# Optimization experiments

Measured on AMD Instinct MI355X. Metric: run time of the kernel, lower is better.

Reference implementation:

```python
import jax, jax.numpy as jnp
import numpy as np

N = 100000   # nodes
E = 1600000  # edges (avg degree 16)
D = 128      # input_dim == output_dim (residual requires equality)
BN_EPS = 1e-5


def setup_inputs() -> dict:
    key = jax.random.key(0)
    ks = jax.random.split(key, 8)
    X = jax.random.normal(ks[0], (N, D), dtype=jnp.float32)
    E_X = jax.random.normal(ks[1], (E, D), dtype=jnp.float32)
    snorm_n = jax.random.uniform(ks[2], (N, 1), dtype=jnp.float32)
    snorm_e = jax.random.uniform(ks[3], (E, 1), dtype=jnp.float32)
    src = jax.random.randint(ks[4], (E,), 0, N, dtype=jnp.int32)
    dst = jax.random.randint(ks[5], (E,), 0, N, dtype=jnp.int32)
    # Linear A and B parameters (torch nn.Linear: y = x @ W.T + b)
    scale = 1.0 / np.sqrt(D)
    A_w = jax.random.uniform(ks[6], (D, D), dtype=jnp.float32, minval=-scale, maxval=scale)
    B_w = jax.random.uniform(ks[7], (D, D), dtype=jnp.float32, minval=-scale, maxval=scale)
    A_b = jnp.zeros((D,), jnp.float32)
    B_b = jnp.zeros((D,), jnp.float32)
    # BatchNorm1d affine params (training mode -> batch stats)
    gamma = jnp.ones((D,), jnp.float32)
    beta = jnp.zeros((D,), jnp.float32)
    return {"X": X, "E_X": E_X, "snorm_n": snorm_n, "snorm_e": snorm_e,
            "src": src, "dst": dst, "A_w": A_w, "A_b": A_b,
            "B_w": B_w, "B_b": B_b, "gamma": gamma, "beta": beta}


def reference(X, E_X, snorm_n, snorm_e, src, dst, A_w, A_b, B_w, B_b, gamma, beta):
    AX = X @ A_w.T + A_b                       # [N, D]
    BX = X @ B_w.T + B_b                       # [N, D]
    # message: gather BX at edge sources; reduce: sum into destinations
    msgs = BX[src]                             # [E, D] irregular gather
    agg = jax.ops.segment_sum(msgs, dst, num_segments=N)  # [N, D]
    # DGL custom reduce only fires for nodes with in-degree > 0;
    # zero-in-degree nodes keep H = X
    indeg = jax.ops.segment_sum(jnp.ones((E,), X.dtype), dst, num_segments=N)
    H = jnp.where(indeg[:, None] > 0, AX + agg, X)
    H = H * snorm_n
    # BatchNorm1d (training mode: biased batch statistics)
    mean = jnp.mean(H, axis=0)
    var = jnp.mean((H - mean) ** 2, axis=0)
    H = (H - mean) * jax.lax.rsqrt(var + BN_EPS) * gamma + beta
    H = jax.nn.relu(H)
    H = X + H                                  # residual
    return (H, E_X)
```

## Files before the change

### kernel.cpp

```cpp
#include <hip/hip_runtime.h>

#define D 128
#define NNODES 100000
#define NEDGES 1600000
#define BN_EPS 1e-5f
#define NB_STATS 2048
#define NBLK_P 391

#define OFF_AX     0
#define OFF_BX16   12800000
#define OFF_ESRC   19200000
#define OFF_ORDER  20800000
#define OFF_INDEG  22400000
#define OFF_ROWS   22510000
#define OFF_LEXC   22620000
#define OFF_BPART  22730000
#define OFF_BSCAN  22731000
#define OFF_PSUM   22740000
#define OFF_PSQ    23010000
#define OFF_SCALE  23280000
#define OFF_SHIFT  23280128
#define WS_NEED_BYTES 93200000ull

#define MAIN_GEMM 512
#define MAIN_EDGE 2048
#define MAIN_AGG  2048
#define MAIN_FIN  2048

#define GEMM_BSZ   24576L
#define GEMM_TOTAL (512L * GEMM_BSZ)
#define HIST_BSZ   3072L
#define HIST_START GEMM_TOTAL
#define HIST_TOTAL (2048L * HIST_BSZ)
#define FILL_START (HIST_START + HIST_TOTAL)
#define FILL_TOTAL (2048L * HIST_BSZ)
#define TAIL_START (FILL_START + FILL_TOTAL)
#define C_TOTAL    51200000L

static __device__ __forceinline__ unsigned short f2bf(float f) {
    unsigned int u = __float_as_uint(f);
    u = (u + 0x7FFF + ((u >> 16) & 1)) >> 16;
    return (unsigned short)u;
}
static __device__ __forceinline__ float bf_lo(unsigned v) {
    return __uint_as_float(v << 16);
}
static __device__ __forceinline__ float bf_hi(unsigned v) {
    return __uint_as_float(v & 0xFFFF0000u);
}

__global__ __launch_bounds__(256, 2) void gemm2_kernel(
    const float* __restrict__ X,
    const float* __restrict__ Aw, const float* __restrict__ Ab,
    const float* __restrict__ Bw, const float* __restrict__ Bb,
    float* __restrict__ AX, unsigned short* __restrict__ BX16,
    const float4* __restrict__ exs, float4* __restrict__ exd,
    long bsz)
{
    const bool isB = (blockIdx.x & 1);
    const float* __restrict__ W    = isB ? Bw : Aw;
    const float* __restrict__ bias = isB ? Bb : Ab;

    long cur  = (long)blockIdx.x * bsz + threadIdx.x;
    const long bend = (long)blockIdx.x * bsz + bsz;

    __shared__ float Ws[D * 132];
    const float4* W4 = (const float4*)W;
    for (int i = threadIdx.x; i < D * D / 4; i += 256) {
        int d  = i >> 5;
        int k4 = i & 31;
        float4 w = W4[i];
        *(float4*)&Ws[d * 132 + 4 * k4] = w;
    }
    __syncthreads();

    const int rg = threadIdx.x >> 5;
    const int cg = threadIdx.x & 31;

    float b[4];
#pragma unroll
    for (int j = 0; j < 4; ++j) b[j] = bias[cg + 32 * j];

    const int ntiles = NNODES / 32;
    for (int t = (blockIdx.x >> 1); t < ntiles; t += (MAIN_GEMM >> 1)) {
        const int row0 = t * 32 + rg * 4;
        float acc[4][4];
#pragma unroll
        for (int r = 0; r < 4; ++r)
#pragma unroll
            for (int j = 0; j < 4; ++j) acc[r][j] = b[j];

        const float* xbase = X + (size_t)row0 * D;
#pragma unroll 4
        for (int k = 0; k < D; k += 4) {
            float4 xr[4];
#pragma unroll
            for (int r = 0; r < 4; ++r)
                xr[r] = *(const float4*)&xbase[r * D + k];
            float4 wv[4];
#pragma unroll
            for (int j = 0; j < 4; ++j)
                wv[j] = *(const float4*)&Ws[(cg + 32 * j) * 132 + k];
#pragma unroll
            for (int r = 0; r < 4; ++r)
#pragma unroll
                for (int j = 0; j < 4; ++j)
                    acc[r][j] += xr[r].x * wv[j].x + xr[r].y * wv[j].y +
                                 xr[r].z * wv[j].z + xr[r].w * wv[j].w;
        }
        if (isB) {
#pragma unroll
            for (int r = 0; r < 4; ++r) {
                unsigned short* yrow = BX16 + (size_t)(row0 + r) * D;
#pragma unroll
                for (int j = 0; j < 4; ++j)
                    yrow[cg + 32 * j] = f2bf(acc[r][j]);
            }
        } else {
#pragma unroll
            for (int r = 0; r < 4; ++r) {
                float* yrow = AX + (size_t)(row0 + r) * D;
#pragma unroll
                for (int j = 0; j < 4; ++j) yrow[cg + 32 * j] = acc[r][j];
            }
        }
#pragma unroll
        for (int j = 0; j < 8; ++j) {
            long idx = cur + j * 256;
            if (idx < bend) exd[idx] = exs[idx];
        }
        cur += 2048;
    }
}

__global__ __launch_bounds__(256) void hist_kernel(
    const int* __restrict__ dst, int* __restrict__ indeg,
    int* __restrict__ order,
    const float4* __restrict__ exs, float4* __restrict__ exd,
    long cstart, long cb)
{
    long cur  = cstart + (long)blockIdx.x * cb + threadIdx.x;
    const long bend = cstart + (long)blockIdx.x * cb + cb;
    int e = blockIdx.x * 256 + threadIdx.x;
#pragma unroll 1
    for (int it = 0; it < 4; ++it) {
        if (e < NEDGES) order[e] = atomicAdd(&indeg[dst[e]], 1);
#pragma unroll
        for (int j = 0; j < 4; ++j) {
            long idx = cur + j * 256;
            if (idx < bend) exd[idx] = exs[idx];
        }
        cur += 1024;
        e   += MAIN_EDGE * 256;
    }
}

__global__ __launch_bounds__(256) void scan1_kernel(
    const int* __restrict__ indeg, int* __restrict__ lexc,
    int* __restrict__ bpart)
{
    __shared__ int ls[256];
    const int i = blockIdx.x * 256 + threadIdx.x;
    const int v = (i < NNODES) ? indeg[i] : 0;
    ls[threadIdx.x] = v;
    __syncthreads();
    for (int off = 1; off < 256; off <<= 1) {
        int u = (threadIdx.x >= off) ? ls[threadIdx.x - off] : 0;
        __syncthreads();
        ls[threadIdx.x] += u;
        __syncthreads();
    }
    if (i < NNODES) lexc[i] = ls[threadIdx.x] - v;
    if (threadIdx.x == 255) bpart[blockIdx.x] = ls[255];
}

__global__ __launch_bounds__(512) void scan2_kernel(
    const int* __restrict__ bpart, int* __restrict__ bscan,
    int* __restrict__ rows)
{
    __shared__ int ls[512];
    const int t = threadIdx.x;
    const int v = (t < NBLK_P) ? bpart[t] : 0;
    ls[t] = v;
    __syncthreads();
    for (int off = 1; off < 512; off <<= 1) {
        int u = (t >= off) ? ls[t - off] : 0;
        __syncthreads();
        ls[t] += u;
        __syncthreads();
    }
    if (t < NBLK_P) bscan[t] = ls[t] - v;
    if (t == 0) rows[NNODES] = NEDGES;
}

__global__ __launch_bounds__(256) void scan3_kernel(
    const int* __restrict__ lexc, const int* __restrict__ bscan,
    int* __restrict__ rows)
{
    const int i = blockIdx.x * 256 + threadIdx.x;
    if (i < NNODES) rows[i] = bscan[blockIdx.x] + lexc[i];
}

__global__ __launch_bounds__(256) void fill_kernel(
    const int* __restrict__ src, const int* __restrict__ dst,
    const int* __restrict__ rows, const int* __restrict__ order,
    int* __restrict__ esrc,
    const float4* __restrict__ exs, float4* __restrict__ exd,
    long cstart, long cb)
{
    long cur  = cstart + (long)blockIdx.x * cb + threadIdx.x;
    const long bend = cstart + (long)blockIdx.x * cb + cb;
    int e = blockIdx.x * 256 + threadIdx.x;
#pragma unroll 1
    for (int it = 0; it < 4; ++it) {
        if (e < NEDGES) esrc[rows[dst[e]] + order[e]] = src[e];
#pragma unroll
        for (int j = 0; j < 4; ++j) {
            long idx = cur + j * 256;
            if (idx < bend) exd[idx] = exs[idx];
        }
        cur += 1024;
        e   += MAIN_EDGE * 256;
    }
}

__global__ __launch_bounds__(256, 8) void agg_kernel(
    const float* __restrict__ AX, const unsigned* __restrict__ BX32,
    const float* __restrict__ X, const float* __restrict__ snorm,
    const int* __restrict__ rows, const int* __restrict__ esrc,
    float* __restrict__ Hpre, float* __restrict__ psum,
    float* __restrict__ psq)
{
    const int w    = threadIdx.x >> 6;
    const int lane = threadIdx.x & 63;
    const int c0   = lane * 2;
    float ps0 = 0.f, ps1 = 0.f, q0 = 0.f, q1 = 0.f;

    for (int i = blockIdx.x * 4 + w; i < NNODES; i += MAIN_AGG * 4) {
        const int rs = rows[i];
        const int re = rows[i + 1];
        float ax, ay;
        if (re > rs) {
            float2 a0 = *(const float2*)&AX[(size_t)i * D + c0];
            ax = a0.x; ay = a0.y;
            int e = rs;
            for (; e + 4 <= re; e += 4) {
                const int s0 = esrc[e + 0], s1 = esrc[e + 1];
                const int s2 = esrc[e + 2], s3 = esrc[e + 3];
                const unsigned v0 = BX32[s0 * 64 + lane];
                const unsigned v1 = BX32[s1 * 64 + lane];
                const unsigned v2 = BX32[s2 * 64 + lane];
                const unsigned v3 = BX32[s3 * 64 + lane];
                ax += bf_lo(v0) + bf_lo(v1) + bf_lo(v2) + bf_lo(v3);
                ay += bf_hi(v0) + bf_hi(v1) + bf_hi(v2) + bf_hi(v3);
            }
            for (; e < re; ++e) {
                const unsigned v = BX32[esrc[e] * 64 + lane];
                ax += bf_lo(v);
                ay += bf_hi(v);
            }
        } else {
            float2 x0 = *(const float2*)&X[(size_t)i * D + c0];
            ax = x0.x; ay = x0.y;
        }
        const float sn = snorm[i];
        ax *= sn; ay *= sn;
        *(float2*)&Hpre[(size_t)i * D + c0] = make_float2(ax, ay);
        ps0 += ax; ps1 += ay;
        q0  += ax * ax; q1 += ay * ay;
    }

    __shared__ float sp[4][D], sq[4][D];
    sp[w][c0] = ps0; sp[w][c0 + 1] = ps1;
    sq[w][c0] = q0;  sq[w][c0 + 1] = q1;
    __syncthreads();
    if (threadIdx.x < D) {
        const int c = threadIdx.x;
        psum[blockIdx.x * D + c] = sp[0][c] + sp[1][c] + sp[2][c] + sp[3][c];
        psq [blockIdx.x * D + c] = sq[0][c] + sq[1][c] + sq[2][c] + sq[3][c];
    }
}

__global__ __launch_bounds__(1024) void bnstats_kernel(
    const float* __restrict__ psum, const float* __restrict__ psq,
    const float* __restrict__ gamma, const float* __restrict__ beta,
    float* __restrict__ scale, float* __restrict__ shift)
{
    const int c = threadIdx.x & 127;
    const int g = threadIdx.x >> 7;
    float s = 0.f, q = 0.f;
    for (int b = g; b < NB_STATS; b += 8) {
        s += psum[b * D + c];
        q += psq [b * D + c];
    }
    __shared__ float ls[8][D], lq[8][D];
    ls[g][c] = s;
    lq[g][c] = q;
    __syncthreads();
    if (threadIdx.x < D) {
        float S = 0.f, Q = 0.f;
#pragma unroll
        for (int g2 = 0; g2 < 8; ++g2) { S += ls[g2][c]; Q += lq[g2][c]; }
        const float inv_n = 1.0f / (float)NNODES;
        float mean = S * inv_n;
        float var  = Q * inv_n - mean * mean;
        float sc   = rsqrtf(var + BN_EPS) * gamma[c];
        scale[c] = sc;
        shift[c] = beta[c] - mean * sc;
    }
}

__global__ __launch_bounds__(256) void final_kernel(
    const float* __restrict__ Hpre, const float* __restrict__ X,
    const float* __restrict__ scale, const float* __restrict__ shift,
    float* __restrict__ out)
{
    const int total = NNODES * D / 4;
    for (int i = blockIdx.x * 256 + threadIdx.x; i < total;
         i += MAIN_FIN * 256) {
        float4 h = ((const float4*)Hpre)[i];
        float4 x = ((const float4*)X)[i];
        int d0 = (i * 4) & 127;
        float4 r;
        r.x = x.x + fmaxf(0.f, h.x * scale[d0 + 0] + shift[d0 + 0]);
        r.y = x.y + fmaxf(0.f, h.y * scale[d0 + 1] + shift[d0 + 1]);
        r.z = x.z + fmaxf(0.f, h.z * scale[d0 + 2] + shift[d0 + 2]);
        r.w = x.w + fmaxf(0.f, h.w * scale[d0 + 3] + shift[d0 + 3]);
        ((float4*)out)[i] = r;
    }
}

extern "C" void kernel_launch(void* const* d_in, const int* in_sizes, int n_in,
                              void* d_out, int out_size, void* d_ws, size_t ws_size,
                              hipStream_t stream)
{
    const float* X       = (const float*)d_in[0];
    const float* E_X     = (const float*)d_in[1];
    const float* snorm_n = (const float*)d_in[2];
    const int*   src     = (const int*)d_in[4];
    const int*   dst     = (const int*)d_in[5];
    const float* A_w     = (const float*)d_in[6];
    const float* A_b     = (const float*)d_in[7];
    const float* B_w     = (const float*)d_in[8];
    const float* B_b     = (const float*)d_in[9];
    const float* gamma   = (const float*)d_in[10];
    const float* beta    = (const float*)d_in[11];

    float* out = (float*)d_out;
    const bool use_ws = (ws_size >= WS_NEED_BYTES);
    float* sb = use_ws ? (float*)d_ws : (out + (size_t)NNODES * D);

    float*          AX    = sb + OFF_AX;
    unsigned short* BX16  = (unsigned short*)(sb + OFF_BX16);
    int*            esrc  = (int*)(sb + OFF_ESRC);
    int*            order = (int*)(sb + OFF_ORDER);
    int*            indeg = (int*)(sb + OFF_INDEG);
    int*            rows  = (int*)(sb + OFF_ROWS);
    int*            lexc  = (int*)(sb + OFF_LEXC);
    int*            bpart = (int*)(sb + OFF_BPART);
    int*            bscan = (int*)(sb + OFF_BSCAN);
    float*          psum  = sb + OFF_PSUM;
    float*          psq   = sb + OFF_PSQ;
    float*          scale = sb + OFF_SCALE;
    float*          shift = sb + OFF_SHIFT;

    const float4* exs = (const float4*)E_X;
    float4*       exd = (float4*)(out + (size_t)NNODES * D);

    const long gemm_bsz  = use_ws ? GEMM_BSZ : 0;
    const long edge_cb   = use_ws ? HIST_BSZ : 0;
    const long tail_from = use_ws ? TAIL_START : 0;

    hipMemsetAsync(indeg, 0, NNODES * sizeof(int), stream);

    gemm2_kernel<<<MAIN_GEMM, 256, 0, stream>>>(
        X, A_w, A_b, B_w, B_b, AX, BX16, exs, exd, gemm_bsz);
    hist_kernel<<<MAIN_EDGE, 256, 0, stream>>>(
        dst, indeg, order, exs, exd, HIST_START, edge_cb);
    scan1_kernel<<<NBLK_P, 256, 0, stream>>>(indeg, lexc, bpart);
    scan2_kernel<<<1, 512, 0, stream>>>(bpart, bscan, rows);
    scan3_kernel<<<NBLK_P, 256, 0, stream>>>(lexc, bscan, rows);
    fill_kernel<<<MAIN_EDGE, 256, 0, stream>>>(
        src, dst, rows, order, esrc, exs, exd, FILL_START, edge_cb);
    agg_kernel<<<MAIN_AGG, 256, 0, stream>>>(
        AX, (const unsigned*)BX16, X, snorm_n, rows, esrc, out, psum, psq);
    bnstats_kernel<<<1, 1024, 0, stream>>>(psum, psq, gamma, beta,
                                           scale, shift);
    final_kernel<<<MAIN_FIN, 256, 0, stream>>>(out, X, scale, shift, out);

    hipMemcpyAsync(exd + tail_from, exs + tail_from,
                   (size_t)(C_TOTAL - tail_from) * sizeof(float4),
                   hipMemcpyDeviceToDevice, stream);
}
```

Baseline: 748.8 us.

## Redistribute E_X copy into dedicated blocks across kernels and drop scan3

The pass-through E_X copy no longer runs interleaved inside the GEMM, hist and fill loops. It now uses separate copy-only blocks prepended to the hist, fill, agg and final kernels, so the copy bandwidth overlaps the gather-heavy agg and final phases. The scan3 kernel and the rows array are removed, and row offsets are computed on the fly from bscan, lexc and indeg. This cuts one launch and one pass over the nodes, at the cost of a few extra indexed loads per node and edge. It also changes how much copy work shares each kernel with its compute blocks.

```diff
diff --git a/kernel.cpp b/kernel.cpp
--- a/kernel.cpp
+++ b/kernel.cpp
@@ -12,7 +12,6 @@
 #define OFF_ESRC   19200000
 #define OFF_ORDER  20800000
 #define OFF_INDEG  22400000
-#define OFF_ROWS   22510000
 #define OFF_LEXC   22620000
 #define OFF_BPART  22730000
 #define OFF_BSCAN  22731000
@@ -27,14 +26,15 @@
 #define MAIN_AGG  2048
 #define MAIN_FIN  2048
 
-#define GEMM_BSZ   24576L
-#define GEMM_TOTAL (512L * GEMM_BSZ)
-#define HIST_BSZ   3072L
-#define HIST_START GEMM_TOTAL
-#define HIST_TOTAL (2048L * HIST_BSZ)
-#define FILL_START (HIST_START + HIST_TOTAL)
-#define FILL_TOTAL (2048L * HIST_BSZ)
-#define TAIL_START (FILL_START + FILL_TOTAL)
+#define NCOPY_SM   256
+#define CPB_SM     16000L
+#define NCOPY_AGG  512
+#define CPB_AGG    39000L
+#define HIST_C0    0L
+#define FILL_C0    4096000L
+#define AGG_C0     8192000L
+#define FIN_C0     28160000L
+#define TAIL_C0    32256000L
 #define C_TOTAL    51200000L
 
 static __device__ __forceinline__ unsigned short f2bf(float f) {
@@ -49,20 +49,24 @@
     return __uint_as_float(v & 0xFFFF0000u);
 }
 
+static __device__ __forceinline__ void copy_blk(
+    const float4* __restrict__ s, float4* __restrict__ d,
+    long base, long cnt)
+{
+    const long end = base + cnt;
+    for (long i = base + threadIdx.x; i < end; i += 256)
+        d[i] = s[i];
+}
+
 __global__ __launch_bounds__(256, 2) void gemm2_kernel(
     const float* __restrict__ X,
     const float* __restrict__ Aw, const float* __restrict__ Ab,
     const float* __restrict__ Bw, const float* __restrict__ Bb,
-    float* __restrict__ AX, unsigned short* __restrict__ BX16,
-    const float4* __restrict__ exs, float4* __restrict__ exd,
-    long bsz)
+    float* __restrict__ AX, unsigned short* __restrict__ BX16)
 {
     const bool isB = (blockIdx.x & 1);
     const float* __restrict__ W    = isB ? Bw : Aw;
     const float* __restrict__ bias = isB ? Bb : Ab;
-
-    long cur  = (long)blockIdx.x * bsz + threadIdx.x;
-    const long bend = (long)blockIdx.x * bsz + bsz;
 
     __shared__ float Ws[D * 132];
     const float4* W4 = (const float4*)W;
@@ -124,35 +128,21 @@
                 for (int j = 0; j < 4; ++j) yrow[cg + 32 * j] = acc[r][j];
             }
         }
-#pragma unroll
-        for (int j = 0; j < 8; ++j) {
-            long idx = cur + j * 256;
-            if (idx < bend) exd[idx] = exs[idx];
-        }
-        cur += 2048;
     }
 }
 
 __global__ __launch_bounds__(256) void hist_kernel(
     const int* __restrict__ dst, int* __restrict__ indeg,
     int* __restrict__ order,
-    const float4* __restrict__ exs, float4* __restrict__ exd,
-    long cstart, long cb)
-{
-    long cur  = cstart + (long)blockIdx.x * cb + threadIdx.x;
-    const long bend = cstart + (long)blockIdx.x * cb + cb;
-    int e = blockIdx.x * 256 + threadIdx.x;
-#pragma unroll 1
-    for (int it = 0; it < 4; ++it) {
-        if (e < NEDGES) order[e] = atomicAdd(&indeg[dst[e]], 1);
-#pragma unroll
-        for (int j = 0; j < 4; ++j) {
-            long idx = cur + j * 256;
-            if (idx < bend) exd[idx] = exs[idx];
-        }
-        cur += 1024;
-        e   += MAIN_EDGE * 256;
-    }
+    const float4* __restrict__ exs, float4* __restrict__ exd, long cpb)
+{
+    if (blockIdx.x < NCOPY_SM) {
+        if (cpb) copy_blk(exs, exd, HIST_C0 + (long)blockIdx.x * cpb, cpb);
+        return;
+    }
+    const int b = blockIdx.x - NCOPY_SM;
+    for (int e = b * 256 + threadIdx.x; e < NEDGES; e += MAIN_EDGE * 256)
+        order[e] = atomicAdd(&indeg[dst[e]], 1);
 }
 
 __global__ __launch_bounds__(256) void scan1_kernel(
@@ -175,8 +165,7 @@
 }
 
 __global__ __launch_bounds__(512) void scan2_kernel(
-    const int* __restrict__ bpart, int* __restrict__ bscan,
-    int* __restrict__ rows)
+    const int* __restrict__ bpart, int* __restrict__ bscan)
 {
     __shared__ int ls[512];
     const int t = threadIdx.x;
@@ -190,57 +179,50 @@
         __syncthreads();
     }
     if (t < NBLK_P) bscan[t] = ls[t] - v;
-    if (t == 0) rows[NNODES] = NEDGES;
-}
-
-__global__ __launch_bounds__(256) void scan3_kernel(
-    const int* __restrict__ lexc, const int* __restrict__ bscan,
-    int* __restrict__ rows)
-{
-    const int i = blockIdx.x * 256 + threadIdx.x;
-    if (i < NNODES) rows[i] = bscan[blockIdx.x] + lexc[i];
 }
 
 __global__ __launch_bounds__(256) void fill_kernel(
     const int* __restrict__ src, const int* __restrict__ dst,
-    const int* __restrict__ rows, const int* __restrict__ order,
-    int* __restrict__ esrc,
-    const float4* __restrict__ exs, float4* __restrict__ exd,
-    long cstart, long cb)
-{
-    long cur  = cstart + (long)blockIdx.x * cb + threadIdx.x;
-    const long bend = cstart + (long)blockIdx.x * cb + cb;
-    int e = blockIdx.x * 256 + threadIdx.x;
-#pragma unroll 1
-    for (int it = 0; it < 4; ++it) {
-        if (e < NEDGES) esrc[rows[dst[e]] + order[e]] = src[e];
-#pragma unroll
-        for (int j = 0; j < 4; ++j) {
-            long idx = cur + j * 256;
-            if (idx < bend) exd[idx] = exs[idx];
-        }
-        cur += 1024;
-        e   += MAIN_EDGE * 256;
+    const int* __restrict__ bscan, const int* __restrict__ lexc,
+    const int* __restrict__ order, int* __restrict__ esrc,
+    const float4* __restrict__ exs, float4* __restrict__ exd, long cpb)
+{
+    if (blockIdx.x < NCOPY_SM) {
+        if (cpb) copy_blk(exs, exd, FILL_C0 + (long)blockIdx.x * cpb, cpb);
+        return;
+    }
+    const int b = blockIdx.x - NCOPY_SM;
+    for (int e = b * 256 + threadIdx.x; e < NEDGES; e += MAIN_EDGE * 256) {
+        const int v = dst[e];
+        esrc[bscan[v >> 8] + lexc[v] + order[e]] = src[e];
     }
 }
 
 __global__ __launch_bounds__(256, 8) void agg_kernel(
     const float* __restrict__ AX, const unsigned* __restrict__ BX32,
     const float* __restrict__ X, const float* __restrict__ snorm,
-    const int* __restrict__ rows, const int* __restrict__ esrc,
+    const int* __restrict__ bscan, const int* __restrict__ lexc,
+    const int* __restrict__ indeg, const int* __restrict__ esrc,
     float* __restrict__ Hpre, float* __restrict__ psum,
-    float* __restrict__ psq)
-{
+    float* __restrict__ psq,
+    const float4* __restrict__ exs, float4* __restrict__ exd, long cpb)
+{
+    if (blockIdx.x < NCOPY_AGG) {
+        if (cpb) copy_blk(exs, exd, AGG_C0 + (long)blockIdx.x * cpb, cpb);
+        return;
+    }
+    const int blk  = blockIdx.x - NCOPY_AGG;
     const int w    = threadIdx.x >> 6;
     const int lane = threadIdx.x & 63;
     const int c0   = lane * 2;
     float ps0 = 0.f, ps1 = 0.f, q0 = 0.f, q1 = 0.f;
 
-    for (int i = blockIdx.x * 4 + w; i < NNODES; i += MAIN_AGG * 4) {
-        const int rs = rows[i];
-        const int re = rows[i + 1];
+    for (int i = blk * 4 + w; i < NNODES; i += MAIN_AGG * 4) {
+        const int rs  = bscan[i >> 8] + lexc[i];
+        const int deg = indeg[i];
+        const int re  = rs + deg;
         float ax, ay;
-        if (re > rs) {
+        if (deg > 0) {
             float2 a0 = *(const float2*)&AX[(size_t)i * D + c0];
             ax = a0.x; ay = a0.y;
             int e = rs;
@@ -276,8 +258,8 @@
     __syncthreads();
     if (threadIdx.x < D) {
         const int c = threadIdx.x;
-        psum[blockIdx.x * D + c] = sp[0][c] + sp[1][c] + sp[2][c] + sp[3][c];
-        psq [blockIdx.x * D + c] = sq[0][c] + sq[1][c] + sq[2][c] + sq[3][c];
+        psum[blk * D + c] = sp[0][c] + sp[1][c] + sp[2][c] + sp[3][c];
+        psq [blk * D + c] = sq[0][c] + sq[1][c] + sq[2][c] + sq[3][c];
     }
 }
 
@@ -313,11 +295,16 @@
 __global__ __launch_bounds__(256) void final_kernel(
     const float* __restrict__ Hpre, const float* __restrict__ X,
     const float* __restrict__ scale, const float* __restrict__ shift,
-    float* __restrict__ out)
-{
+    float* __restrict__ out,
+    const float4* __restrict__ exs, float4* __restrict__ exd, long cpb)
+{
+    if (blockIdx.x < NCOPY_SM) {
+        if (cpb) copy_blk(exs, exd, FIN_C0 + (long)blockIdx.x * cpb, cpb);
+        return;
+    }
+    const int b = blockIdx.x - NCOPY_SM;
     const int total = NNODES * D / 4;
-    for (int i = blockIdx.x * 256 + threadIdx.x; i < total;
-         i += MAIN_FIN * 256) {
+    for (int i = b * 256 + threadIdx.x; i < total; i += MAIN_FIN * 256) {
         float4 h = ((const float4*)Hpre)[i];
         float4 x = ((const float4*)X)[i];
         int d0 = (i * 4) & 127;
@@ -355,7 +342,6 @@
     int*            esrc  = (int*)(sb + OFF_ESRC);
     int*            order = (int*)(sb + OFF_ORDER);
     int*            indeg = (int*)(sb + OFF_INDEG);
-    int*            rows  = (int*)(sb + OFF_ROWS);
     int*            lexc  = (int*)(sb + OFF_LEXC);
     int*            bpart = (int*)(sb + OFF_BPART);
     int*            bscan = (int*)(sb + OFF_BSCAN);
@@ -367,26 +353,27 @@
     const float4* exs = (const float4*)E_X;
     float4*       exd = (float4*)(out + (size_t)NNODES * D);
 
-    const long gemm_bsz  = use_ws ? GEMM_BSZ : 0;
-    const long edge_cb   = use_ws ? HIST_BSZ : 0;
-    const long tail_from = use_ws ? TAIL_START : 0;
+    const long cpb_sm   = use_ws ? CPB_SM : 0;
+    const long cpb_agg  = use_ws ? CPB_AGG : 0;
+    const long tail_from = use_ws ? TAIL_C0 : 0;
 
     hipMemsetAsync(indeg, 0, NNODES * sizeof(int), stream);
 
     gemm2_kernel<<<MAIN_GEMM, 256, 0, stream>>>(
-        X, A_w, A_b, B_w, B_b, AX, BX16, exs, exd, gemm_bsz);
-    hist_kernel<<<MAIN_EDGE, 256, 0, stream>>>(
-        dst, indeg, order, exs, exd, HIST_START, edge_cb);
+        X, A_w, A_b, B_w, B_b, AX, BX16);
+    hist_kernel<<<NCOPY_SM + MAIN_EDGE, 256, 0, stream>>>(
+        dst, indeg, order, exs, exd, cpb_sm);
     scan1_kernel<<<NBLK_P, 256, 0, stream>>>(indeg, lexc, bpart);
-    scan2_kernel<<<1, 512, 0, stream>>>(bpart, bscan, rows);
-    scan3_kernel<<<NBLK_P, 256, 0, stream>>>(lexc, bscan, rows);
-    fill_kernel<<<MAIN_EDGE, 256, 0, stream>>>(
-        src, dst, rows, order, esrc, exs, exd, FILL_START, edge_cb);
-    agg_kernel<<<MAIN_AGG, 256, 0, stream>>>(
-        AX, (const unsigned*)BX16, X, snorm_n, rows, esrc, out, psum, psq);
+    scan2_kernel<<<1, 512, 0, stream>>>(bpart, bscan);
+    fill_kernel<<<NCOPY_SM + MAIN_EDGE, 256, 0, stream>>>(
+        src, dst, bscan, lexc, order, esrc, exs, exd, cpb_sm);
+    agg_kernel<<<NCOPY_AGG + MAIN_AGG, 256, 0, stream>>>(
+        AX, (const unsigned*)BX16, X, snorm_n, bscan, lexc, indeg, esrc,
+        out, psum, psq, exs, exd, cpb_agg);
     bnstats_kernel<<<1, 1024, 0, stream>>>(psum, psq, gamma, beta,
                                            scale, shift);
-    final_kernel<<<MAIN_FIN, 256, 0, stream>>>(out, X, scale, shift, out);
+    final_kernel<<<NCOPY_SM + MAIN_FIN, 256, 0, stream>>>(
+        out, X, scale, shift, out, exs, exd, cpb_sm);
 
     hipMemcpyAsync(exd + tail_from, exs + tail_from,
                    (size_t)(C_TOTAL - tail_from) * sizeof(float4),
```

After: 812.1 us. 8.4% more time.
